# Kernel optimization log

Measured on AMD Instinct MI355X. Metric: run time of the kernel, lower is better.

## Reference

```python
import jax, jax.numpy as jnp
import numpy as np

DIM = 128
HOP = 2
NEIGH = [12, 2]  # neighbor_num per hop
ALPHA = 0.2      # leaky-relu slope
NUM_NODE = 50000
B, S = 128, 50
STDV = 1.0 / np.sqrt(DIM)


def _leaky(x):
    return jnp.where(x >= 0, x, ALPHA * x)


def _local_agg(h, adj, a_local):
    # h: [B,S,D], adj: [B,S,S] ints in 0..4, a_local: [4,D]
    a_in = h[:, :, None, :] * h[:, None, :, :]            # [B,S,S,D]
    e = _leaky(jnp.einsum('bijd,kd->kbij', a_in, a_local))  # [4,B,S,S]
    att = jnp.full(adj.shape, -9e15, dtype=h.dtype)
    for k in range(4):
        att = jnp.where(adj == k + 1, e[k], att)
    att = jax.nn.softmax(att, axis=-1)
    return jnp.einsum('bij,bjd->bid', att, h)


def _global_agg(self_v, neigh_v, extra_v, w1, w2, w3, bias):
    # self_v: [B,N,D], neigh_v: [B,N,K,D], extra_v: [B,N,D]
    a = _leaky(jnp.einsum('bnkd,de->bnke', extra_v[:, :, None, :] * neigh_v, w1))
    a = jnp.einsum('bnke,e->bnk', a, w2)
    a = jax.nn.softmax(a, axis=-1)
    agg = jnp.einsum('bnk,bnkd->bnd', a, neigh_v)
    out = jnp.concatenate([self_v, agg], axis=-1) @ w3 + bias
    return jax.nn.relu(out)


def setup_inputs() -> dict:
    key = jax.random.key(0)
    ks = jax.random.split(key, 12)
    u = lambda k, shp: jax.random.uniform(k, shp, jnp.float32, -STDV, STDV)
    return {
        'inputs': jax.random.randint(ks[0], (B, S), 0, NUM_NODE),
        'adj': jax.random.randint(ks[1], (B, S, S), 0, 5),
        'mask_item': jnp.ones((B, S), dtype=jnp.int32),
        'item': jax.random.randint(ks[2], (B, S), 0, NUM_NODE),
        'first_adj': jax.random.randint(ks[3], (B, S * NEIGH[0]), 0, NUM_NODE),
        'adj_all': jax.random.randint(ks[4], (NUM_NODE, 2), 0, NUM_NODE),
        'embedding': u(ks[5], (NUM_NODE, DIM)),
        'a_local': u(ks[6], (4, DIM)),
        'gw1': u(ks[7], (HOP, DIM, DIM)),
        'gw2': u(ks[8], (HOP, DIM)),
        'gw3': u(ks[9], (HOP, 2 * DIM, DIM)),
        'gbias': u(ks[10], (HOP, DIM)),
    }


def reference(inputs, adj, mask_item, item, first_adj, adj_all,
              embedding, a_local, gw1, gw2, gw3, gbias):
    b, s = inputs.shape
    h = embedding[inputs]                                  # [B,S,D]
    h_local = _local_agg(h, adj, a_local)

    m = mask_item.astype(embedding.dtype)[..., None]       # [B,S,1]
    item_emb = embedding[item] * m
    sum_item = jnp.sum(item_emb, 1) / jnp.sum(m, 1)        # [B,D]
    sess = sum_item[:, None, :]                            # [B,1,D]

    # multi-hop neighbor sampling
    neigh1 = first_adj.reshape(b, s * NEIGH[0])            # [B, 600]
    neigh2 = adj_all[neigh1.reshape(-1)].reshape(b, s * NEIGH[0] * NEIGH[1])  # [B,1200]
    ev = [embedding[inputs], embedding[neigh1], embedding[neigh2]]

    for n_hop in range(HOP):
        nxt = []
        for hop in range(HOP - n_hop):
            neigh_v = ev[hop + 1].reshape(b, -1, NEIGH[hop], DIM)
            extra_v = jnp.broadcast_to(sess, (b, ev[hop].shape[1], DIM))
            nxt.append(_global_agg(ev[hop], neigh_v, extra_v,
                                   gw1[n_hop], gw2[n_hop], gw3[n_hop], gbias[n_hop]))
        ev = nxt
    h_global = ev[0].reshape(b, s, DIM)

    # dropout is identity at eval
    return h_local + h_global
```

## Files before the change

kernel.cpp:

```cpp
#include <hip/hip_runtime.h>
#include <stdint.h>

typedef unsigned short ushort_t;
typedef __attribute__((ext_vector_type(8))) short bf16x8;
typedef __attribute__((ext_vector_type(4))) float f32x4;

#define B_   128
#define S_   50
#define D_   128
#define ALPHA_ 0.2f

__device__ __forceinline__ float bf2f(ushort_t u){
  return __uint_as_float(((uint32_t)u) << 16);
}
__device__ __forceinline__ ushort_t f2bf(float f){
  uint32_t x = __float_as_uint(f);
  x = (x + 0x7fffu + ((x >> 16) & 1u)) >> 16;
  return (ushort_t)x;
}
__device__ __forceinline__ float leaky(float x){ return x >= 0.f ? x : ALPHA_*x; }

__device__ __forceinline__ int detect_flag_block(const uint32_t* __restrict__ emb_raw){
  __shared__ int flg;
  if (threadIdx.x == 0){
    int ok = 1;
    for (int i = 0; i < 64; i++){
      uint32_t lo = emb_raw[i] & 0xffffu;
      uint32_t ex = (lo >> 7) & 0xFFu;
      if (!(lo == 0u || (ex >= 64u && ex <= 126u))) ok = 0;
    }
    flg = ok;
  }
  __syncthreads();
  return flg;
}

#define NLOCAL_ 512
#define NSESS_  64
#define NTPREP_ 1564
#define NCVT_   6347
#define NPREP_  48
#define TPREP_BASE_ (NLOCAL_ + NSESS_)
#define CVT_BASE_   (TPREP_BASE_ + NTPREP_)
#define PREP_BASE_  (CVT_BASE_ + NCVT_)
#define K1_GRID_    (PREP_BASE_ + NPREP_)

__global__ __launch_bounds__(256) void k1(
    const int* __restrict__ inputs, const int* __restrict__ adj,
    const int* __restrict__ item, const int* __restrict__ mask,
    const void* __restrict__ p0, const void* __restrict__ p1,
    const void* __restrict__ p2, const void* __restrict__ p3,
    const void* __restrict__ p4, const void* __restrict__ p5,
    ushort_t* __restrict__ emb_b, uint4* __restrict__ w1f, uint4* __restrict__ w3f,
    ushort_t* __restrict__ sessb, ushort_t* __restrict__ hlb,
    ushort_t* __restrict__ Tt, ushort_t* __restrict__ Tb)
{
  __shared__ uint4 smem[2048];
  int blk = blockIdx.x, tid = threadIdx.x;
  int flag = detect_flag_block((const uint32_t*)p0);

  if (blk < NLOCAL_){
    ushort_t* hSp   = (ushort_t*)smem;
    float*    attSp = (float*)((char*)smem + 17408);
    int*      sidsp = (int*)((char*)smem + 21760);
    ushort_t* alSp  = (ushort_t*)((char*)smem + 22016);
    int b  = blk >> 2;
    int mi = blk & 3;
    if (tid < 64) sidsp[tid] = (tid < S_) ? inputs[b*S_ + tid] : 0;
    for (int i = tid; i < 512; i += 256)
      alSp[i] = flag ? ((const ushort_t*)p1)[i] : f2bf(((const float*)p1)[i]);
    __syncthreads();
    if (flag){
      const ushort_t* e16 = (const ushort_t*)p0;
      for (int idx = tid; idx < 64*16; idx += 256){
        int j = idx >> 4, ch = idx & 15;
        uint4 v = {0u, 0u, 0u, 0u};
        if (j < S_) v = *(const uint4*)(e16 + (size_t)sidsp[j]*D_ + ch*8);
        *(uint4*)(hSp + j*136 + ch*8) = v;
      }
    } else {
      const float* ef = (const float*)p0;
      for (int idx = tid; idx < 64*32; idx += 256){
        int j = idx >> 5, ch = idx & 31;
        union { ushort_t u[4]; uint2 d2; } o;
        o.d2 = make_uint2(0u, 0u);
        if (j < S_){
          float4 v = *(const float4*)(ef + (size_t)sidsp[j]*D_ + ch*4);
          o.u[0]=f2bf(v.x); o.u[1]=f2bf(v.y); o.u[2]=f2bf(v.z); o.u[3]=f2bf(v.w);
        }
        *(uint2*)(hSp + j*136 + ch*4) = o.d2;
      }
    }
    for (int idx = tid; idx < 16*64; idx += 256)
      attSp[(idx >> 6)*68 + (idx & 63)] = -9.0e15f;
    __syncthreads();

    int lane = tid & 63, wv = tid >> 6;
    int q = lane >> 4, c = lane & 15;

    f32x4 Eacc[4];
    #pragma unroll
    for (int ni = 0; ni < 4; ni++) Eacc[ni] = (f32x4){0.f,0.f,0.f,0.f};
    #pragma unroll
    for (int kt = 0; kt < 4; kt++){
      uint4 av = *(const uint4*)(alSp + wv*D_ + kt*32 + q*8);
      const uint32_t* ap = (const uint32_t*)&av;
      uint4 hv = *(const uint4*)(hSp + (mi*16 + c)*136 + kt*32 + q*8);
      const uint32_t* hp = (const uint32_t*)&hv;
      union { ushort_t u[8]; bf16x8 v; } afr;
      #pragma unroll
      for (int p = 0; p < 4; p++){
        float x0 = __uint_as_float(hp[p] << 16)         * __uint_as_float(ap[p] << 16);
        float x1 = __uint_as_float(hp[p] & 0xffff0000u) * __uint_as_float(ap[p] & 0xffff0000u);
        afr.u[2*p]   = f2bf(x0);
        afr.u[2*p+1] = f2bf(x1);
      }
      #pragma unroll
      for (int ni = 0; ni < 4; ni++){
        union { uint4 q4; bf16x8 v; } bfr;
        bfr.q4 = *(const uint4*)(hSp + (ni*16 + c)*136 + kt*32 + q*8);
        Eacc[ni] = __builtin_amdgcn_mfma_f32_16x16x32_bf16(afr.v, bfr.v, Eacc[ni], 0,0,0);
      }
    }
    const int* adjb = adj + (size_t)b*S_*S_;
    #pragma unroll
    for (int ni = 0; ni < 4; ni++){
      int j = ni*16 + c;
      #pragma unroll
      for (int r = 0; r < 4; r++){
        int i = mi*16 + q*4 + r;
        if (i < S_ && j < S_){
          int kk = adjb[i*S_ + j];
          if (kk == wv + 1) attSp[(q*4 + r)*68 + j] = leaky(Eacc[ni][r]);
        }
      }
    }
    __syncthreads();
    {
      int r  = tid >> 4;
      int cg = tid & 15;
      int i  = mi*16 + r;
      float v0 = attSp[r*68 + cg*4+0], v1 = attSp[r*68 + cg*4+1];
      float v2 = attSp[r*68 + cg*4+2], v3 = attSp[r*68 + cg*4+3];
      float mx = fmaxf(fmaxf(v0,v1), fmaxf(v2,v3));
      #pragma unroll
      for (int off = 1; off < 16; off <<= 1) mx = fmaxf(mx, __shfl_xor(mx, off, 16));
      float e0 = (cg*4+0 < S_) ? __expf(v0 - mx) : 0.f;
      float e1 = (cg*4+1 < S_) ? __expf(v1 - mx) : 0.f;
      float e2 = (cg*4+2 < S_) ? __expf(v2 - mx) : 0.f;
      float e3 = (cg*4+3 < S_) ? __expf(v3 - mx) : 0.f;
      float s = e0 + e1 + e2 + e3;
      #pragma unroll
      for (int off = 1; off < 16; off <<= 1) s += __shfl_xor(s, off, 16);
      float inv = (i < S_) ? 1.f / s : 0.f;
      attSp[r*68 + cg*4+0] = e0*inv;
      attSp[r*68 + cg*4+1] = e1*inv;
      attSp[r*68 + cg*4+2] = e2*inv;
      attSp[r*68 + cg*4+3] = e3*inv;
    }
    __syncthreads();
    f32x4 Pacc[2];
    Pacc[0] = (f32x4){0.f,0.f,0.f,0.f};
    Pacc[1] = (f32x4){0.f,0.f,0.f,0.f};
    #pragma unroll
    for (int kt = 0; kt < 2; kt++){
      union { ushort_t u[8]; bf16x8 v; } afr;
      const float* arow = attSp + c*68 + kt*32 + q*8;
      #pragma unroll
      for (int j = 0; j < 8; j++) afr.u[j] = f2bf(arow[j]);
      #pragma unroll
      for (int nn = 0; nn < 2; nn++){
        int ni = 2*wv + nn;
        union { ushort_t u[8]; bf16x8 v; } bfr;
        #pragma unroll
        for (int jj = 0; jj < 8; jj++)
          bfr.u[jj] = hSp[(kt*32 + q*8 + jj)*136 + ni*16 + c];
        Pacc[nn] = __builtin_amdgcn_mfma_f32_16x16x32_bf16(afr.v, bfr.v, Pacc[nn], 0,0,0);
      }
    }
    #pragma unroll
    for (int nn = 0; nn < 2; nn++){
      int d = (2*wv + nn)*16 + c;
      #pragma unroll
      for (int r = 0; r < 4; r++){
        int i = mi*16 + q*4 + r;
        if (i < S_) hlb[((size_t)b*S_ + i)*D_ + d] = f2bf(Pacc[nn][r]);
      }
    }
  } else if (blk < NLOCAL_ + NSESS_){
    int b = (blk - NLOCAL_)*2 + (tid >> 7);
    int d = tid & 127;
    float acc = 0.f, den = 0.f;
    if (flag){
      const ushort_t* e16 = (const ushort_t*)p0;
      for (int s = 0; s < S_; s++){
        float fm = (float)mask[b*S_ + s];
        int id = item[b*S_ + s];
        acc += fm * bf2f(e16[(size_t)id*D_ + d]);
        den += fm;
      }
    } else {
      const float* ef = (const float*)p0;
      for (int s = 0; s < S_; s++){
        float fm = (float)mask[b*S_ + s];
        int id = item[b*S_ + s];
        acc += fm * ef[(size_t)id*D_ + d];
        den += fm;
      }
    }
    sessb[b*D_ + d] = f2bf(acc / den);
  } else if (blk < CVT_BASE_){
    if (!Tt) return;
    int tp   = blk - TPREP_BASE_;
    int half = tp & 1;
    int rowbase = (tp >> 1) * 64;
    for (int i = tid; i < 2048; i += 256){
      int kt = i >> 9, rem = i & 511, t = rem >> 6, ln = rem & 63;
      int q = ln >> 4, c = ln & 15;
      union { ushort_t u[8]; uint4 q4; } e;
      #pragma unroll
      for (int j = 0; j < 8; j++){
        int idx = (32*(half*4 + kt) + q*8 + j)*128 + 16*t + c;
        e.u[j] = flag ? ((const ushort_t*)p4)[idx] : f2bf(((const float*)p4)[idx]);
      }
      smem[i] = e.q4;
    }
    __syncthreads();
    int lane = tid & 63, wave = tid >> 6;
    int m = lane & 15, q = lane >> 4;
    int row = rowbase + wave*16 + m;
    int rowc = row < 50000 ? row : 49999;
    f32x4 acc[8];
    #pragma unroll
    for (int t = 0; t < 8; t++) acc[t] = (f32x4){0.f,0.f,0.f,0.f};
    #pragma unroll
    for (int kt = 0; kt < 4; kt++){
      union { ushort_t u[8]; uint4 q4; bf16x8 v; } bfr;
      if (flag){
        bfr.q4 = *(const uint4*)((const ushort_t*)p0 + (size_t)rowc*D_ + kt*32 + q*8);
      } else {
        const float* ef = (const float*)p0 + (size_t)rowc*D_ + kt*32 + q*8;
        float4 f0 = *(const float4*)(ef);
        float4 f1 = *(const float4*)(ef + 4);
        bfr.u[0]=f2bf(f0.x); bfr.u[1]=f2bf(f0.y); bfr.u[2]=f2bf(f0.z); bfr.u[3]=f2bf(f0.w);
        bfr.u[4]=f2bf(f1.x); bfr.u[5]=f2bf(f1.y); bfr.u[6]=f2bf(f1.z); bfr.u[7]=f2bf(f1.w);
      }
      #pragma unroll
      for (int t = 0; t < 8; t++){
        union { uint4 q4; bf16x8 v; } af;
        af.q4 = smem[(kt*8 + t)*64 + lane];
        acc[t] = __builtin_amdgcn_mfma_f32_16x16x32_bf16(af.v, bfr.v, acc[t], 0, 0, 0);
      }
    }
    if (row < 50000){
      ushort_t* dst = (half ? Tb : Tt) + (size_t)row*D_;
      #pragma unroll
      for (int t = 0; t < 8; t++){
        int col0 = 16*t + q*4;
        union { ushort_t u[4]; uint2 d2; } pk;
        #pragma unroll
        for (int r = 0; r < 4; r++) pk.u[r] = f2bf(acc[t][r]);
        *(uint2*)(dst + col0) = pk.d2;
      }
    }
  } else if (blk < PREP_BASE_){
    const int seg_end[6] = {6400000, 6400512, 6433280, 6433536, 6499072, 6499328};
    int base = ((blk - CVT_BASE_)*256 + tid) * 4;
    if (base >= 6499328) return;
    int s = 0;
    while (base >= seg_end[s]) s++;
    int segbase = (s == 0) ? 0 : seg_end[s-1];
    const void* src = (s==0)?p0:(s==1)?p1:(s==2)?p2:(s==3)?p3:(s==4)?p4:p5;
    int off = base - segbase;
    union { ushort_t u[4]; uint2 d2; } o;
    if (flag){
      o.d2 = *(const uint2*)((const ushort_t*)src + off);
    } else {
      float4 v = *(const float4*)((const float*)src + off);
      o.u[0] = f2bf(v.x); o.u[1] = f2bf(v.y); o.u[2] = f2bf(v.z); o.u[3] = f2bf(v.w);
    }
    *(uint2*)(emb_b + base) = o.d2;
  } else {
    int id = (blk - PREP_BASE_)*256 + tid;
    if (id >= 12288) return;
    if (id < 4096){
      int h = id >> 11, i = id & 2047;
      int kt = i >> 9, rem = i & 511, t = rem >> 6, ln = rem & 63;
      int q = ln >> 4, c = ln & 15;
      union { ushort_t u[8]; uint4 q4; } e;
      #pragma unroll
      for (int j = 0; j < 8; j++){
        int idx = h*16384 + (32*kt + q*8 + j)*128 + 16*t + c;
        e.u[j] = flag ? ((const ushort_t*)p2)[idx] : f2bf(((const float*)p2)[idx]);
      }
      w1f[h*2048 + i] = e.q4;
    } else {
      int id2 = id - 4096;
      int h = id2 >> 12, i = id2 & 4095;
      int kt = i >> 9, rem = i & 511, t = rem >> 6, ln = rem & 63;
      int q = ln >> 4, c = ln & 15;
      union { ushort_t u[8]; uint4 q4; } e;
      #pragma unroll
      for (int j = 0; j < 8; j++){
        int idx = h*32768 + (32*kt + q*8 + j)*128 + 16*t + c;
        e.u[j] = flag ? ((const ushort_t*)p4)[idx] : f2bf(((const float*)p4)[idx]);
      }
      w3f[h*4096 + i] = e.q4;
    }
  }
}

__global__ __launch_bounds__(256) void score2_ab(
    const ushort_t* __restrict__ sessb, const ushort_t* __restrict__ emb,
    const int* __restrict__ neigh1, const int* __restrict__ adj_all,
    const uint4* __restrict__ w1f, const ushort_t* __restrict__ w2,
    float* __restrict__ score)
{
  __shared__ uint4 bfrag[2048];
  __shared__ ushort_t sS[128];
  int blk = blockIdx.x, tid = threadIdx.x;
  int sb  = blk / 6;
  int sub = blk - sb*6;
  int grp = sub >> 1;
  int halft = sub & 1;
  if (tid < 16) ((uint4*)sS)[tid] = ((const uint4*)(sessb + (size_t)sb*D_))[tid];
  __syncthreads();
  for (int i = tid; i < 2048; i += 256){
    int kt = i >> 9, ln = i & 63, q = (ln >> 4);
    uint4 w = w1f[i];
    uint4 sv = *(const uint4*)(sS + kt*32 + q*8);
    const ushort_t* wu = (const ushort_t*)&w;
    const ushort_t* su = (const ushort_t*)&sv;
    union { ushort_t u[8]; uint4 q4; } o;
    #pragma unroll
    for (int j = 0; j < 8; j++) o.u[j] = f2bf(bf2f(wu[j]) * bf2f(su[j]));
    bfrag[i] = o.q4;
  }
  __syncthreads();
  int lane = tid & 63, wave = tid >> 6;
  int m = lane & 15, q = lane >> 4;
  float w2v[8];
  #pragma unroll
  for (int t = 0; t < 8; t++) w2v[t] = bf2f(w2[16*t + m]);

  int tend = halft ? 38 : 19;
  for (int t = halft*19 + wave; t < tend; t += 4){
    int rr = t*16 + m;
    int rrc = rr < 599 ? rr : 599;
    int nid;
    if (grp == 0){
      nid = neigh1[sb*600 + rrc];
    } else {
      int r2 = sb*1200 + (grp-1)*600 + rrc;
      nid = adj_all[(size_t)neigh1[r2 >> 1]*2 + (r2 & 1)];
    }
    const ushort_t* nrow = emb + (size_t)nid*D_;
    f32x4 acc[8];
    #pragma unroll
    for (int t8 = 0; t8 < 8; t8++) acc[t8] = (f32x4){0.f,0.f,0.f,0.f};
    #pragma unroll
    for (int kt = 0; kt < 4; kt++){
      union { uint4 q4; bf16x8 v; } af;
      af.q4 = *(const uint4*)(nrow + kt*32 + q*8);
      #pragma unroll
      for (int t8 = 0; t8 < 8; t8++){
        union { uint4 q4; bf16x8 v; } bf;
        bf.q4 = bfrag[(kt*8 + t8)*64 + lane];
        acc[t8] = __builtin_amdgcn_mfma_f32_16x16x32_bf16(af.v, bf.v, acc[t8], 0, 0, 0);
      }
    }
    #pragma unroll
    for (int r = 0; r < 4; r++){
      float s = 0.f;
      #pragma unroll
      for (int t8 = 0; t8 < 8; t8++) s += leaky(acc[t8][r]) * w2v[t8];
      s += __shfl_xor(s, 1, 64);
      s += __shfl_xor(s, 2, 64);
      s += __shfl_xor(s, 4, 64);
      s += __shfl_xor(s, 8, 64);
      if (m == 0){
        int rw = t*16 + q*4 + r;
        if (rw < 600){
          int sidx = (grp == 0) ? (sb*600 + rw)
                                : (76800 + sb*1200 + (grp-1)*600 + rw);
          score[sidx] = s;
        }
      }
    }
  }
}

__global__ __launch_bounds__(256) void score2_c(
    const ushort_t* __restrict__ sessb, const ushort_t* __restrict__ out1,
    const uint4* __restrict__ w1f, const ushort_t* __restrict__ w2,
    float* __restrict__ score)
{
  __shared__ uint4 bfrag[2048];
  __shared__ ushort_t sS[128];
  int blk = blockIdx.x, tid = threadIdx.x;
  int sb  = blk >> 2;
  int qtr = blk & 3;
  if (tid < 16) ((uint4*)sS)[tid] = ((const uint4*)(sessb + (size_t)sb*D_))[tid];
  __syncthreads();
  for (int i = tid; i < 2048; i += 256){
    int kt = i >> 9, ln = i & 63, q = (ln >> 4);
    uint4 w = w1f[i];
    uint4 sv = *(const uint4*)(sS + kt*32 + q*8);
    const ushort_t* wu = (const ushort_t*)&w;
    const ushort_t* su = (const ushort_t*)&sv;
    union { ushort_t u[8]; uint4 q4; } o;
    #pragma unroll
    for (int j = 0; j < 8; j++) o.u[j] = f2bf(bf2f(wu[j]) * bf2f(su[j]));
    bfrag[i] = o.q4;
  }
  __syncthreads();
  int lane = tid & 63, wave = tid >> 6;
  int m = lane & 15, q = lane >> 4;
  float w2v[8];
  #pragma unroll
  for (int t = 0; t < 8; t++) w2v[t] = bf2f(w2[16*t + m]);

  int t0 = qtr*10, tend = (qtr*10 + 10 < 38) ? qtr*10 + 10 : 38;
  for (int t = t0 + wave; t < tend; t += 4){
    int rr = t*16 + m;
    int rrc = rr < 599 ? rr : 599;
    const ushort_t* nrow = out1 + ((size_t)sb*600 + rrc)*D_;
    f32x4 acc[8];
    #pragma unroll
    for (int t8 = 0; t8 < 8; t8++) acc[t8] = (f32x4){0.f,0.f,0.f,0.f};
    #pragma unroll
    for (int kt = 0; kt < 4; kt++){
      union { uint4 q4; bf16x8 v; } af;
      af.q4 = *(const uint4*)(nrow + kt*32 + q*8);
      #pragma unroll
      for (int t8 = 0; t8 < 8; t8++){
        union { uint4 q4; bf16x8 v; } bf;
        bf.q4 = bfrag[(kt*8 + t8)*64 + lane];
        acc[t8] = __builtin_amdgcn_mfma_f32_16x16x32_bf16(af.v, bf.v, acc[t8], 0, 0, 0);
      }
    }
    #pragma unroll
    for (int r = 0; r < 4; r++){
      float s = 0.f;
      #pragma unroll
      for (int t8 = 0; t8 < 8; t8++) s += leaky(acc[t8][r]) * w2v[t8];
      s += __shfl_xor(s, 1, 64);
      s += __shfl_xor(s, 2, 64);
      s += __shfl_xor(s, 4, 64);
      s += __shfl_xor(s, 8, 64);
      if (m == 0){
        int rw = t*16 + q*4 + r;
        if (rw < 600) score[sb*600 + rw] = s;
      }
    }
  }
}

template<int K>
__device__ __forceinline__ void softmaxK(const float* __restrict__ sc, float att[K]){
  float mx = -__builtin_inff();
  #pragma unroll
  for (int k = 0; k < K; k++){ att[k] = sc[k]; mx = fmaxf(mx, att[k]); }
  float s = 0.f;
  #pragma unroll
  for (int k = 0; k < K; k++){ att[k] = __expf(att[k] - mx); s += att[k]; }
  float inv = 1.f / s;
  #pragma unroll
  for (int k = 0; k < K; k++) att[k] *= inv;
}

template<int K>
__device__ __forceinline__ void out_tile(
    int lane, const uint4* __restrict__ afrag,
    const ushort_t* __restrict__ sptr, const ushort_t* const nptr[K],
    const float att[K], f32x4 acc[8]){
  int q = lane >> 4;
  #pragma unroll
  for (int kt = 0; kt < 8; kt++){
    union { ushort_t u[8]; uint4 q4; bf16x8 v; } bfr;
    if (kt < 4){
      bfr.q4 = *(const uint4*)(sptr + kt*32 + q*8);
    } else {
      float g[8] = {0,0,0,0,0,0,0,0};
      #pragma unroll
      for (int k = 0; k < K; k++){
        uint4 nv = *(const uint4*)(nptr[k] + (kt-4)*32 + q*8);
        const uint32_t* np = (const uint32_t*)&nv;
        #pragma unroll
        for (int p = 0; p < 4; p++){
          g[2*p]   = fmaf(att[k], __uint_as_float(np[p] << 16),         g[2*p]);
          g[2*p+1] = fmaf(att[k], __uint_as_float(np[p] & 0xffff0000u), g[2*p+1]);
        }
      }
      #pragma unroll
      for (int j = 0; j < 8; j++) bfr.u[j] = f2bf(g[j]);
    }
    #pragma unroll
    for (int t = 0; t < 8; t++){
      union { uint4 q4; bf16x8 v; } af;
      af.q4 = afrag[(kt*8 + t)*64 + lane];
      acc[t] = __builtin_amdgcn_mfma_f32_16x16x32_bf16(af.v, bfr.v, acc[t], 0, 0, 0);
    }
  }
}

__global__ __launch_bounds__(256) void gather_out(
    const int* __restrict__ idx, const int* __restrict__ nbr,
    const int* __restrict__ adj_all, const float* __restrict__ score,
    const ushort_t* __restrict__ Tt, const ushort_t* __restrict__ Tb,
    const ushort_t* __restrict__ bias,
    ushort_t* __restrict__ o0c, ushort_t* __restrict__ out1c,
    int nA50, int nTot, int scoreBbase)
{
  int row  = (blockIdx.x*256 + threadIdx.x) >> 6;
  int lane = threadIdx.x & 63;
  if (row >= nTot) return;
  row = __builtin_amdgcn_readfirstlane(row);
  float b0 = bf2f(bias[lane*2]), b1 = bf2f(bias[lane*2 + 1]);
  float acc0, acc1;
  ushort_t* dst;
  if (row < nA50){
    float att[12];
    softmaxK<12>(score + (size_t)row*12, att);
    uint32_t sv = *(const uint32_t*)(Tt + (size_t)idx[row]*D_ + lane*2);
    acc0 = __uint_as_float(sv << 16);
    acc1 = __uint_as_float(sv & 0xffff0000u);
    #pragma unroll
    for (int k = 0; k < 12; k++){
      uint32_t nv = *(const uint32_t*)(Tb + (size_t)nbr[row*12 + k]*D_ + lane*2);
      acc0 = fmaf(att[k], __uint_as_float(nv << 16),          acc0);
      acc1 = fmaf(att[k], __uint_as_float(nv & 0xffff0000u),  acc1);
    }
    dst = o0c + (size_t)row*D_;
  } else {
    int rB = row - nA50;
    float att[2];
    softmaxK<2>(score + scoreBbase + (size_t)rB*2, att);
    int self = nbr[rB];
    uint32_t sv = *(const uint32_t*)(Tt + (size_t)self*D_ + lane*2);
    acc0 = __uint_as_float(sv << 16);
    acc1 = __uint_as_float(sv & 0xffff0000u);
    #pragma unroll
    for (int k = 0; k < 2; k++){
      uint32_t nv = *(const uint32_t*)(Tb + (size_t)adj_all[(size_t)self*2 + k]*D_ + lane*2);
      acc0 = fmaf(att[k], __uint_as_float(nv << 16),          acc0);
      acc1 = fmaf(att[k], __uint_as_float(nv & 0xffff0000u),  acc1);
    }
    dst = out1c + (size_t)rB*D_;
  }
  union { ushort_t u[2]; uint32_t d; } pk;
  pk.u[0] = f2bf(fmaxf(acc0 + b0, 0.f));
  pk.u[1] = f2bf(fmaxf(acc1 + b1, 0.f));
  *(uint32_t*)(dst + lane*2) = pk.d;
}

__global__ __launch_bounds__(256) void out_mfma_c2(
    const float* __restrict__ score, const ushort_t* __restrict__ out1,
    const ushort_t* __restrict__ selfsrc, const uint4* __restrict__ w3f,
    const ushort_t* __restrict__ bias,
    const ushort_t* __restrict__ addsrc, float* __restrict__ outf, int nrows){
  __shared__ uint4 afrag[4096];
  int tid = threadIdx.x;
  for (int i = tid; i < 4096; i += 256) afrag[i] = w3f[i];
  __syncthreads();
  int lane = tid & 63, wave = tid >> 6;
  int mrow = lane & 15, q = lane >> 4;
  float bv[8][4];
  #pragma unroll
  for (int t = 0; t < 8; t++){
    const ushort_t* bp = bias + 16*t + q*4;
    #pragma unroll
    for (int r = 0; r < 4; r++) bv[t][r] = bf2f(bp[r]);
  }
  int row_base = blockIdx.x*64 + wave*16;
  int row = row_base + mrow;
  bool active = row < nrows;
  int rowc = active ? row : (nrows - 1);
  const ushort_t* sptr = selfsrc + (size_t)rowc*D_;
  const ushort_t* nptr[12];
  #pragma unroll
  for (int k = 0; k < 12; k++) nptr[k] = out1 + (size_t)(rowc*12 + k)*D_;
  float att[12];
  softmaxK<12>(score + (size_t)rowc*12, att);
  f32x4 acc[8];
  #pragma unroll
  for (int t = 0; t < 8; t++) acc[t] = (f32x4){0.f,0.f,0.f,0.f};
  out_tile<12>(lane, afrag, sptr, nptr, att, acc);
  if (active){
    #pragma unroll
    for (int t = 0; t < 8; t++){
      int col0 = 16*t + q*4;
      float v[4];
      const ushort_t* ap = addsrc + (size_t)row*D_ + col0;
      #pragma unroll
      for (int r = 0; r < 4; r++)
        v[r] = fmaxf(acc[t][r] + bv[t][r], 0.f) + bf2f(ap[r]);
      *(f32x4*)(outf + (size_t)row*D_ + col0) = (f32x4){v[0], v[1], v[2], v[3]};
    }
  }
}

__global__ __launch_bounds__(256) void score_mfma_ab(
    const ushort_t* __restrict__ sessb, const ushort_t* __restrict__ emb,
    const int* __restrict__ neigh1, const int* __restrict__ adj_all,
    const uint4* __restrict__ w1f, const ushort_t* __restrict__ w2,
    float* __restrict__ score, int nA){
  __shared__ uint4 bfrag[2048];
  int tid = threadIdx.x;
  for (int i = tid; i < 2048; i += 256) bfrag[i] = w1f[i];
  __syncthreads();
  int lane = tid & 63, wave = tid >> 6;
  int m = lane & 15, q = lane >> 4;
  float w2v[8];
  #pragma unroll
  for (int t = 0; t < 8; t++) w2v[t] = bf2f(w2[16*t + m]);

  for (int it = 0; it < 2; it++){
    int row_base = blockIdx.x*128 + it*64 + wave*16;
    int row = row_base + m;
    const ushort_t* nrow; int b;
    if (row < nA){
      nrow = emb + (size_t)neigh1[row]*D_;
      b = row / 600;
    } else {
      int r2 = row - nA;
      nrow = emb + (size_t)adj_all[(size_t)neigh1[r2>>1]*2 + (r2&1)]*D_;
      b = r2 / 1200;
    }
    const ushort_t* srow = sessb + (size_t)b*D_;

    f32x4 acc[8];
    #pragma unroll
    for (int t = 0; t < 8; t++) acc[t] = (f32x4){0.f,0.f,0.f,0.f};
    #pragma unroll
    for (int kt = 0; kt < 4; kt++){
      uint4 nv = *(const uint4*)(nrow + kt*32 + q*8);
      uint4 sv = *(const uint4*)(srow + kt*32 + q*8);
      const uint32_t* np = (const uint32_t*)&nv;
      const uint32_t* sp = (const uint32_t*)&sv;
      union { ushort_t u[8]; bf16x8 v; } afr;
      #pragma unroll
      for (int p = 0; p < 4; p++){
        uint32_t n2 = np[p], s2 = sp[p];
        float a0 = __uint_as_float(n2 << 16)          * __uint_as_float(s2 << 16);
        float a1 = __uint_as_float(n2 & 0xffff0000u)  * __uint_as_float(s2 & 0xffff0000u);
        afr.u[2*p]   = f2bf(a0);
        afr.u[2*p+1] = f2bf(a1);
      }
      #pragma unroll
      for (int t = 0; t < 8; t++){
        union { uint4 q4; bf16x8 v; } bfr;
        bfr.q4 = bfrag[(kt*8 + t)*64 + lane];
        acc[t] = __builtin_amdgcn_mfma_f32_16x16x32_bf16(afr.v, bfr.v, acc[t], 0, 0, 0);
      }
    }
    #pragma unroll
    for (int r = 0; r < 4; r++){
      float s = 0.f;
      #pragma unroll
      for (int t = 0; t < 8; t++) s += leaky(acc[t][r]) * w2v[t];
      s += __shfl_xor(s, 1, 64);
      s += __shfl_xor(s, 2, 64);
      s += __shfl_xor(s, 4, 64);
      s += __shfl_xor(s, 8, 64);
      if (m == 0) score[row_base + q*4 + r] = s;
    }
  }
}

__global__ __launch_bounds__(256) void score_mfma_c(
    const ushort_t* __restrict__ sessb, const ushort_t* __restrict__ out1,
    const uint4* __restrict__ w1f, const ushort_t* __restrict__ w2,
    float* __restrict__ score){
  __shared__ uint4 bfrag[2048];
  int tid = threadIdx.x;
  for (int i = tid; i < 2048; i += 256) bfrag[i] = w1f[i];
  __syncthreads();
  int lane = tid & 63, wave = tid >> 6;
  int m = lane & 15, q = lane >> 4;
  float w2v[8];
  #pragma unroll
  for (int t = 0; t < 8; t++) w2v[t] = bf2f(w2[16*t + m]);
  for (int it = 0; it < 2; it++){
    int row_base = blockIdx.x*128 + it*64 + wave*16;
    int row = row_base + m;
    const ushort_t* nrow = out1 + (size_t)row*D_;
    int b = row / 600;
    const ushort_t* srow = sessb + (size_t)b*D_;
    f32x4 acc[8];
    #pragma unroll
    for (int t = 0; t < 8; t++) acc[t] = (f32x4){0.f,0.f,0.f,0.f};
    #pragma unroll
    for (int kt = 0; kt < 4; kt++){
      uint4 nv = *(const uint4*)(nrow + kt*32 + q*8);
      uint4 sv = *(const uint4*)(srow + kt*32 + q*8);
      const uint32_t* np = (const uint32_t*)&nv;
      const uint32_t* sp = (const uint32_t*)&sv;
      union { ushort_t u[8]; bf16x8 v; } afr;
      #pragma unroll
      for (int p = 0; p < 4; p++){
        uint32_t n2 = np[p], s2 = sp[p];
        float a0 = __uint_as_float(n2 << 16)          * __uint_as_float(s2 << 16);
        float a1 = __uint_as_float(n2 & 0xffff0000u)  * __uint_as_float(s2 & 0xffff0000u);
        afr.u[2*p]   = f2bf(a0);
        afr.u[2*p+1] = f2bf(a1);
      }
      #pragma unroll
      for (int t = 0; t < 8; t++){
        union { uint4 q4; bf16x8 v; } bfr;
        bfr.q4 = bfrag[(kt*8 + t)*64 + lane];
        acc[t] = __builtin_amdgcn_mfma_f32_16x16x32_bf16(afr.v, bfr.v, acc[t], 0, 0, 0);
      }
    }
    #pragma unroll
    for (int r = 0; r < 4; r++){
      float s = 0.f;
      #pragma unroll
      for (int t = 0; t < 8; t++) s += leaky(acc[t][r]) * w2v[t];
      s += __shfl_xor(s, 1, 64);
      s += __shfl_xor(s, 2, 64);
      s += __shfl_xor(s, 4, 64);
      s += __shfl_xor(s, 8, 64);
      if (m == 0) score[row_base + q*4 + r] = s;
    }
  }
}

__global__ __launch_bounds__(512) void out_mfma_ab(
    const float* __restrict__ score, const int* __restrict__ idx,
    const int* __restrict__ nbr, const int* __restrict__ adj_all,
    const ushort_t* __restrict__ emb, const uint4* __restrict__ w3f,
    const ushort_t* __restrict__ bias,
    ushort_t* __restrict__ o0c, ushort_t* __restrict__ out1c,
    int nA, int nTot, int scoreBbase){
  __shared__ uint4 afrag[4096];
  int tid = threadIdx.x;
  for (int i = tid; i < 4096; i += 512) afrag[i] = w3f[i];
  __syncthreads();
  int lane = tid & 63, wave = tid >> 6;
  int mrow = lane & 15, q = lane >> 4;
  float bv[8][4];
  #pragma unroll
  for (int t = 0; t < 8; t++){
    const ushort_t* bp = bias + 16*t + q*4;
    #pragma unroll
    for (int r = 0; r < 4; r++) bv[t][r] = bf2f(bp[r]);
  }
  int row_base = blockIdx.x*128 + wave*16;
  int row = row_base + mrow;
  bool active = row < nTot;
  int rowc = active ? row : (nTot - 1);
  bool isA = rowc < nA;
  f32x4 acc[8];
  #pragma unroll
  for (int t = 0; t < 8; t++) acc[t] = (f32x4){0.f,0.f,0.f,0.f};
  if (isA){
    const ushort_t* sptr = emb + (size_t)idx[rowc]*D_;
    const ushort_t* nptr[12];
    #pragma unroll
    for (int k = 0; k < 12; k++) nptr[k] = emb + (size_t)nbr[rowc*12 + k]*D_;
    float att[12];
    softmaxK<12>(score + (size_t)rowc*12, att);
    out_tile<12>(lane, afrag, sptr, nptr, att, acc);
  } else {
    int rB = rowc - nA;
    const ushort_t* sptr = emb + (size_t)nbr[rB]*D_;
    const ushort_t* nptr[2];
    #pragma unroll
    for (int k = 0; k < 2; k++) nptr[k] = emb + (size_t)adj_all[(size_t)nbr[rB]*2 + k]*D_;
    float att[2];
    softmaxK<2>(score + scoreBbase + (size_t)rB*2, att);
    out_tile<2>(lane, afrag, sptr, nptr, att, acc);
  }
  if (active){
    ushort_t* dst = isA ? (o0c + (size_t)row*D_) : (out1c + (size_t)(row - nA)*D_);
    #pragma unroll
    for (int t = 0; t < 8; t++){
      int col0 = 16*t + q*4;
      union { ushort_t u[4]; uint2 d2; } pk;
      #pragma unroll
      for (int r = 0; r < 4; r++) pk.u[r] = f2bf(fmaxf(acc[t][r] + bv[t][r], 0.f));
      *(uint2*)(dst + col0) = pk.d2;
    }
  }
}

__global__ __launch_bounds__(512) void out_mfma_c(
    const float* __restrict__ score, const ushort_t* __restrict__ out1,
    const ushort_t* __restrict__ selfsrc, const uint4* __restrict__ w3f,
    const ushort_t* __restrict__ bias,
    const ushort_t* __restrict__ addsrc, float* __restrict__ outf, int nrows){
  __shared__ uint4 afrag[4096];
  int tid = threadIdx.x;
  for (int i = tid; i < 4096; i += 512) afrag[i] = w3f[i];
  __syncthreads();
  int lane = tid & 63, wave = tid >> 6;
  int mrow = lane & 15, q = lane >> 4;
  float bv[8][4];
  #pragma unroll
  for (int t = 0; t < 8; t++){
    const ushort_t* bp = bias + 16*t + q*4;
    #pragma unroll
    for (int r = 0; r < 4; r++) bv[t][r] = bf2f(bp[r]);
  }
  int row_base = blockIdx.x*128 + wave*16;
  int row = row_base + mrow;
  bool active = row < nrows;
  int rowc = active ? row : (nrows - 1);
  const ushort_t* sptr = selfsrc + (size_t)rowc*D_;
  const ushort_t* nptr[12];
  #pragma unroll
  for (int k = 0; k < 12; k++) nptr[k] = out1 + (size_t)(rowc*12 + k)*D_;
  float att[12];
  softmaxK<12>(score + (size_t)rowc*12, att);
  f32x4 acc[8];
  #pragma unroll
  for (int t = 0; t < 8; t++) acc[t] = (f32x4){0.f,0.f,0.f,0.f};
  out_tile<12>(lane, afrag, sptr, nptr, att, acc);
  if (active){
    #pragma unroll
    for (int t = 0; t < 8; t++){
      int col0 = 16*t + q*4;
      float v[4];
      const ushort_t* ap = addsrc + (size_t)row*D_ + col0;
      #pragma unroll
      for (int r = 0; r < 4; r++)
        v[r] = fmaxf(acc[t][r] + bv[t][r], 0.f) + bf2f(ap[r]);
      *(f32x4*)(outf + (size_t)row*D_ + col0) = (f32x4){v[0], v[1], v[2], v[3]};
    }
  }
}

extern "C" void kernel_launch(void* const* d_in, const int* in_sizes, int n_in,
                              void* d_out, int out_size, void* d_ws, size_t ws_size,
                              hipStream_t stream) {
  const int* inputs    = (const int*)d_in[0];
  const int* adj       = (const int*)d_in[1];
  const int* mask_item = (const int*)d_in[2];
  const int* item      = (const int*)d_in[3];
  const int* first_adj = (const int*)d_in[4];
  const int* adj_all   = (const int*)d_in[5];

  char* ws = (char*)d_ws;
  size_t o = 0;
  ushort_t* emb_b  = (ushort_t*)(ws + o); o += 12800000;
  ushort_t* alocb  = (ushort_t*)(ws + o); o += 1024;
  ushort_t* gw1b   = (ushort_t*)(ws + o); o += 65536;
  ushort_t* gw2b   = (ushort_t*)(ws + o); o += 512;
  ushort_t* gw3b   = (ushort_t*)(ws + o); o += 131072;
  ushort_t* gbb    = (ushort_t*)(ws + o); o += 512;
  ushort_t* sessb  = (ushort_t*)(ws + o); o += 32768;
  ushort_t* hlb    = (ushort_t*)(ws + o); o += 1638400;
  uint4*    w1f    = (uint4*)(ws + o);    o += 65536;
  uint4*    w3f    = (uint4*)(ws + o);    o += 131072;
  size_t fixed = o;
  (void)alocb; (void)gw1b; (void)gw3b;

  float* outp = (float*)d_out;

  const size_t TPATH_NEED = fixed + 2*(size_t)12800000
                          + (size_t)128*153600
                          + (size_t)128*12800
                          + (size_t)3*128*600*4;
  bool tpath = (ws_size >= TPATH_NEED);

  ushort_t* Tt = nullptr; ushort_t* Tb = nullptr;
  if (tpath){
    Tt = (ushort_t*)(ws + o);  o += 12800000;
    Tb = (ushort_t*)(ws + o);  o += 12800000;
  }

  k1<<<K1_GRID_, 256, 0, stream>>>(
      inputs, adj, item, mask_item,
      d_in[6], d_in[7], d_in[8], d_in[9], d_in[10], d_in[11],
      emb_b, w1f, w3f, sessb, hlb, Tt, Tb);

  if (tpath){
    ushort_t* out1c = (ushort_t*)(ws + o);  o += (size_t)128*153600;
    ushort_t* o0c   = (ushort_t*)(ws + o);  o += (size_t)128*12800;
    float*    score = (float*)(ws + o);
    int nA600 = 128*600, nA50 = 128*50, nTot = 128*650;

    score2_ab<<<768, 256, 0, stream>>>(sessb, emb_b, first_adj, adj_all,
                                       w1f, gw2b, score);
    gather_out<<<(nTot*64 + 255)/256, 256, 0, stream>>>(inputs, first_adj, adj_all, score,
                                                        Tt, Tb, gbb, o0c, out1c,
                                                        nA50, nTot, nA600);
    score2_c<<<512, 256, 0, stream>>>(sessb, out1c, w1f + 2048, gw2b + 128, score);
    out_mfma_c2<<<(nA50 + 63)/64, 256, 0, stream>>>(score, out1c, o0c,
                                                    w3f + 4096, gbb + 128,
                                                    hlb, outp, nA50);
  } else {
    int CHB = 16;
    if      (ws_size >= fixed + (size_t)128*173600) CHB = 128;
    else if (ws_size >= fixed + (size_t)64 *173600) CHB = 64;
    else if (ws_size >= fixed + (size_t)32 *173600) CHB = 32;
    ushort_t* out1c = (ushort_t*)(ws + o);  o += (size_t)CHB*153600;
    ushort_t* o0c   = (ushort_t*)(ws + o);  o += (size_t)CHB*12800;
    float*    score = (float*)(ws + o);

    int nchunk = B_ / CHB;
    for (int c = 0; c < nchunk; c++){
      int b0 = c * CHB;
      const int* fadj  = first_adj + (size_t)b0 * 600;
      const ushort_t* sbc = sessb + (size_t)b0 * D_;
      ushort_t*  hlc   = hlb  + (size_t)b0 * 50 * D_;
      float*     outc  = outp + (size_t)b0 * 50 * D_;
      int nA600 = CHB*600, nA50 = CHB*50, nTot = CHB*650;

      score_mfma_ab<<<(3*nA600)/128, 256, 0, stream>>>(sbc, emb_b, fadj, adj_all,
                                                       w1f, gw2b, score, nA600);
      out_mfma_ab<<<(nTot + 127)/128, 512, 0, stream>>>(score, inputs + b0*50, fadj, adj_all,
                                                        emb_b, w3f, gbb, o0c, out1c,
                                                        nA50, nTot, nA600);
      score_mfma_c<<<nA600/128, 256, 0, stream>>>(sbc, out1c, w1f + 2048, gw2b + 128, score);
      out_mfma_c<<<(nA50 + 127)/128, 512, 0, stream>>>(score, out1c, o0c,
                                                       w3f + 4096, gbb + 128,
                                                       hlc, outc, nA50);
    }
  }
}
```

Before: 222.8 us.

## Move table-transform blocks into second kernel using prepacked bf16 weights and embedding

Moves the per-row embedding×W3 table precompute (Tt/Tb) out of the first fused kernel and into a new second kernel alongside the score blocks. In its new place it reads the already-converted bf16 embedding and the pre-packed w3 fragments, so it no longer reformats weights or converts fp32 per block. The conversion blocks now process 8 elements per thread with 128-bit loads, which halves the number of conversion blocks. Shared memory in the local-attention blocks becomes statically sized arrays, which may reduce per-block LDS for those blocks. In exchange, the table pass now has to wait until the whole first kernel has finished.

After: 195.4 us. -12.3%, faster.

```diff
diff --git a/kernel.cpp b/kernel.cpp
--- a/kernel.cpp
+++ b/kernel.cpp
@@ -37,11 +37,9 @@
 
 #define NLOCAL_ 512
 #define NSESS_  64
-#define NTPREP_ 1564
-#define NCVT_   6347
+#define NCVT_   3174
 #define NPREP_  48
-#define TPREP_BASE_ (NLOCAL_ + NSESS_)
-#define CVT_BASE_   (TPREP_BASE_ + NTPREP_)
+#define CVT_BASE_   (NLOCAL_ + NSESS_)
 #define PREP_BASE_  (CVT_BASE_ + NCVT_)
 #define K1_GRID_    (PREP_BASE_ + NPREP_)
 
@@ -52,31 +50,29 @@
     const void* __restrict__ p2, const void* __restrict__ p3,
     const void* __restrict__ p4, const void* __restrict__ p5,
     ushort_t* __restrict__ emb_b, uint4* __restrict__ w1f, uint4* __restrict__ w3f,
-    ushort_t* __restrict__ sessb, ushort_t* __restrict__ hlb,
-    ushort_t* __restrict__ Tt, ushort_t* __restrict__ Tb)
+    ushort_t* __restrict__ sessb, ushort_t* __restrict__ hlb)
 {
-  __shared__ uint4 smem[2048];
   int blk = blockIdx.x, tid = threadIdx.x;
   int flag = detect_flag_block((const uint32_t*)p0);
 
   if (blk < NLOCAL_){
-    ushort_t* hSp   = (ushort_t*)smem;
-    float*    attSp = (float*)((char*)smem + 17408);
-    int*      sidsp = (int*)((char*)smem + 21760);
-    ushort_t* alSp  = (ushort_t*)((char*)smem + 22016);
+    __shared__ ushort_t hS[64][136];
+    __shared__ float    attS[16][68];
+    __shared__ int      sids[64];
+    __shared__ ushort_t alS[512];
     int b  = blk >> 2;
     int mi = blk & 3;
-    if (tid < 64) sidsp[tid] = (tid < S_) ? inputs[b*S_ + tid] : 0;
+    if (tid < 64) sids[tid] = (tid < S_) ? inputs[b*S_ + tid] : 0;
     for (int i = tid; i < 512; i += 256)
-      alSp[i] = flag ? ((const ushort_t*)p1)[i] : f2bf(((const float*)p1)[i]);
+      alS[i] = flag ? ((const ushort_t*)p1)[i] : f2bf(((const float*)p1)[i]);
     __syncthreads();
     if (flag){
       const ushort_t* e16 = (const ushort_t*)p0;
       for (int idx = tid; idx < 64*16; idx += 256){
         int j = idx >> 4, ch = idx & 15;
         uint4 v = {0u, 0u, 0u, 0u};
-        if (j < S_) v = *(const uint4*)(e16 + (size_t)sidsp[j]*D_ + ch*8);
-        *(uint4*)(hSp + j*136 + ch*8) = v;
+        if (j < S_) v = *(const uint4*)(e16 + (size_t)sids[j]*D_ + ch*8);
+        *(uint4*)(&hS[j][ch*8]) = v;
       }
     } else {
       const float* ef = (const float*)p0;
@@ -85,14 +81,14 @@
         union { ushort_t u[4]; uint2 d2; } o;
         o.d2 = make_uint2(0u, 0u);
         if (j < S_){
-          float4 v = *(const float4*)(ef + (size_t)sidsp[j]*D_ + ch*4);
+          float4 v = *(const float4*)(ef + (size_t)sids[j]*D_ + ch*4);
           o.u[0]=f2bf(v.x); o.u[1]=f2bf(v.y); o.u[2]=f2bf(v.z); o.u[3]=f2bf(v.w);
         }
-        *(uint2*)(hSp + j*136 + ch*4) = o.d2;
+        *(uint2*)(&hS[j][ch*4]) = o.d2;
       }
     }
     for (int idx = tid; idx < 16*64; idx += 256)
-      attSp[(idx >> 6)*68 + (idx & 63)] = -9.0e15f;
+      attS[idx >> 6][idx & 63] = -9.0e15f;
     __syncthreads();
 
     int lane = tid & 63, wv = tid >> 6;
@@ -103,9 +99,9 @@
     for (int ni = 0; ni < 4; ni++) Eacc[ni] = (f32x4){0.f,0.f,0.f,0.f};
     #pragma unroll
     for (int kt = 0; kt < 4; kt++){
-      uint4 av = *(const uint4*)(alSp + wv*D_ + kt*32 + q*8);
+      uint4 av = *(const uint4*)(alS + wv*D_ + kt*32 + q*8);
       const uint32_t* ap = (const uint32_t*)&av;
-      uint4 hv = *(const uint4*)(hSp + (mi*16 + c)*136 + kt*32 + q*8);
+      uint4 hv = *(const uint4*)(&hS[mi*16 + c][kt*32 + q*8]);
       const uint32_t* hp = (const uint32_t*)&hv;
       union { ushort_t u[8]; bf16x8 v; } afr;
       #pragma unroll
@@ -118,7 +114,7 @@
       #pragma unroll
       for (int ni = 0; ni < 4; ni++){
         union { uint4 q4; bf16x8 v; } bfr;
-        bfr.q4 = *(const uint4*)(hSp + (ni*16 + c)*136 + kt*32 + q*8);
+        bfr.q4 = *(const uint4*)(&hS[ni*16 + c][kt*32 + q*8]);
         Eacc[ni] = __builtin_amdgcn_mfma_f32_16x16x32_bf16(afr.v, bfr.v, Eacc[ni], 0,0,0);
       }
     }
@@ -131,7 +127,7 @@
         int i = mi*16 + q*4 + r;
         if (i < S_ && j < S_){
           int kk = adjb[i*S_ + j];
-          if (kk == wv + 1) attSp[(q*4 + r)*68 + j] = leaky(Eacc[ni][r]);
+          if (kk == wv + 1) attS[q*4 + r][j] = leaky(Eacc[ni][r]);
         }
       }
     }
@@ -140,8 +136,8 @@
       int r  = tid >> 4;
       int cg = tid & 15;
       int i  = mi*16 + r;
-      float v0 = attSp[r*68 + cg*4+0], v1 = attSp[r*68 + cg*4+1];
-      float v2 = attSp[r*68 + cg*4+2], v3 = attSp[r*68 + cg*4+3];
+      float v0 = attS[r][cg*4+0], v1 = attS[r][cg*4+1];
+      float v2 = attS[r][cg*4+2], v3 = attS[r][cg*4+3];
       float mx = fmaxf(fmaxf(v0,v1), fmaxf(v2,v3));
       #pragma unroll
       for (int off = 1; off < 16; off <<= 1) mx = fmaxf(mx, __shfl_xor(mx, off, 16));
@@ -153,10 +149,10 @@
       #pragma unroll
       for (int off = 1; off < 16; off <<= 1) s += __shfl_xor(s, off, 16);
       float inv = (i < S_) ? 1.f / s : 0.f;
-      attSp[r*68 + cg*4+0] = e0*inv;
-      attSp[r*68 + cg*4+1] = e1*inv;
-      attSp[r*68 + cg*4+2] = e2*inv;
-      attSp[r*68 + cg*4+3] = e3*inv;
+      attS[r][cg*4+0] = e0*inv;
+      attS[r][cg*4+1] = e1*inv;
+      attS[r][cg*4+2] = e2*inv;
+      attS[r][cg*4+3] = e3*inv;
     }
     __syncthreads();
     f32x4 Pacc[2];
@@ -165,7 +161,7 @@
     #pragma unroll
     for (int kt = 0; kt < 2; kt++){
       union { ushort_t u[8]; bf16x8 v; } afr;
-      const float* arow = attSp + c*68 + kt*32 + q*8;
+      const float* arow = &attS[c][kt*32 + q*8];
       #pragma unroll
       for (int j = 0; j < 8; j++) afr.u[j] = f2bf(arow[j]);
       #pragma unroll
@@ -174,7 +170,7 @@
         union { ushort_t u[8]; bf16x8 v; } bfr;
         #pragma unroll
         for (int jj = 0; jj < 8; jj++)
-          bfr.u[jj] = hSp[(kt*32 + q*8 + jj)*136 + ni*16 + c];
+          bfr.u[jj] = hS[kt*32 + q*8 + jj][ni*16 + c];
         Pacc[nn] = __builtin_amdgcn_mfma_f32_16x16x32_bf16(afr.v, bfr.v, Pacc[nn], 0,0,0);
       }
     }
@@ -187,7 +183,7 @@
         if (i < S_) hlb[((size_t)b*S_ + i)*D_ + d] = f2bf(Pacc[nn][r]);
       }
     }
-  } else if (blk < NLOCAL_ + NSESS_){
+  } else if (blk < CVT_BASE_){
     int b = (blk - NLOCAL_)*2 + (tid >> 7);
     int d = tid & 127;
     float acc = 0.f, den = 0.f;
@@ -209,77 +205,26 @@
       }
     }
     sessb[b*D_ + d] = f2bf(acc / den);
-  } else if (blk < CVT_BASE_){
-    if (!Tt) return;
-    int tp   = blk - TPREP_BASE_;
-    int half = tp & 1;
-    int rowbase = (tp >> 1) * 64;
-    for (int i = tid; i < 2048; i += 256){
-      int kt = i >> 9, rem = i & 511, t = rem >> 6, ln = rem & 63;
-      int q = ln >> 4, c = ln & 15;
-      union { ushort_t u[8]; uint4 q4; } e;
-      #pragma unroll
-      for (int j = 0; j < 8; j++){
-        int idx = (32*(half*4 + kt) + q*8 + j)*128 + 16*t + c;
-        e.u[j] = flag ? ((const ushort_t*)p4)[idx] : f2bf(((const float*)p4)[idx]);
-      }
-      smem[i] = e.q4;
-    }
-    __syncthreads();
-    int lane = tid & 63, wave = tid >> 6;
-    int m = lane & 15, q = lane >> 4;
-    int row = rowbase + wave*16 + m;
-    int rowc = row < 50000 ? row : 49999;
-    f32x4 acc[8];
-    #pragma unroll
-    for (int t = 0; t < 8; t++) acc[t] = (f32x4){0.f,0.f,0.f,0.f};
-    #pragma unroll
-    for (int kt = 0; kt < 4; kt++){
-      union { ushort_t u[8]; uint4 q4; bf16x8 v; } bfr;
-      if (flag){
-        bfr.q4 = *(const uint4*)((const ushort_t*)p0 + (size_t)rowc*D_ + kt*32 + q*8);
-      } else {
-        const float* ef = (const float*)p0 + (size_t)rowc*D_ + kt*32 + q*8;
-        float4 f0 = *(const float4*)(ef);
-        float4 f1 = *(const float4*)(ef + 4);
-        bfr.u[0]=f2bf(f0.x); bfr.u[1]=f2bf(f0.y); bfr.u[2]=f2bf(f0.z); bfr.u[3]=f2bf(f0.w);
-        bfr.u[4]=f2bf(f1.x); bfr.u[5]=f2bf(f1.y); bfr.u[6]=f2bf(f1.z); bfr.u[7]=f2bf(f1.w);
-      }
-      #pragma unroll
-      for (int t = 0; t < 8; t++){
-        union { uint4 q4; bf16x8 v; } af;
-        af.q4 = smem[(kt*8 + t)*64 + lane];
-        acc[t] = __builtin_amdgcn_mfma_f32_16x16x32_bf16(af.v, bfr.v, acc[t], 0, 0, 0);
-      }
-    }
-    if (row < 50000){
-      ushort_t* dst = (half ? Tb : Tt) + (size_t)row*D_;
-      #pragma unroll
-      for (int t = 0; t < 8; t++){
-        int col0 = 16*t + q*4;
-        union { ushort_t u[4]; uint2 d2; } pk;
-        #pragma unroll
-        for (int r = 0; r < 4; r++) pk.u[r] = f2bf(acc[t][r]);
-        *(uint2*)(dst + col0) = pk.d2;
-      }
-    }
   } else if (blk < PREP_BASE_){
     const int seg_end[6] = {6400000, 6400512, 6433280, 6433536, 6499072, 6499328};
-    int base = ((blk - CVT_BASE_)*256 + tid) * 4;
+    int base = ((blk - CVT_BASE_)*256 + tid) * 8;
     if (base >= 6499328) return;
     int s = 0;
     while (base >= seg_end[s]) s++;
     int segbase = (s == 0) ? 0 : seg_end[s-1];
     const void* src = (s==0)?p0:(s==1)?p1:(s==2)?p2:(s==3)?p3:(s==4)?p4:p5;
     int off = base - segbase;
-    union { ushort_t u[4]; uint2 d2; } o;
+    union { ushort_t u[8]; uint4 q4; } o;
     if (flag){
-      o.d2 = *(const uint2*)((const ushort_t*)src + off);
+      o.q4 = *(const uint4*)((const ushort_t*)src + off);
     } else {
-      float4 v = *(const float4*)((const float*)src + off);
-      o.u[0] = f2bf(v.x); o.u[1] = f2bf(v.y); o.u[2] = f2bf(v.z); o.u[3] = f2bf(v.w);
-    }
-    *(uint2*)(emb_b + base) = o.d2;
+      const float* fp = (const float*)src + off;
+      float4 v0 = *(const float4*)(fp);
+      float4 v1 = *(const float4*)(fp + 4);
+      o.u[0]=f2bf(v0.x); o.u[1]=f2bf(v0.y); o.u[2]=f2bf(v0.z); o.u[3]=f2bf(v0.w);
+      o.u[4]=f2bf(v1.x); o.u[5]=f2bf(v1.y); o.u[6]=f2bf(v1.z); o.u[7]=f2bf(v1.w);
+    }
+    *(uint4*)(emb_b + base) = o.q4;
   } else {
     int id = (blk - PREP_BASE_)*256 + tid;
     if (id >= 12288) return;
@@ -310,17 +255,62 @@
   }
 }
 
-__global__ __launch_bounds__(256) void score2_ab(
-    const ushort_t* __restrict__ sessb, const ushort_t* __restrict__ emb,
+#define NT2TPREP_ 1564
+#define NT2SCORE_ 768
+#define K2_GRID_  (NT2TPREP_ + NT2SCORE_)
+
+__global__ __launch_bounds__(256) void k2(
+    const ushort_t* __restrict__ emb, const uint4* __restrict__ w3f,
+    ushort_t* __restrict__ Tt, ushort_t* __restrict__ Tb,
+    const ushort_t* __restrict__ sessb,
     const int* __restrict__ neigh1, const int* __restrict__ adj_all,
     const uint4* __restrict__ w1f, const ushort_t* __restrict__ w2,
     float* __restrict__ score)
 {
-  __shared__ uint4 bfrag[2048];
+  __shared__ uint4 frag[2048];
   __shared__ ushort_t sS[128];
   int blk = blockIdx.x, tid = threadIdx.x;
-  int sb  = blk / 6;
-  int sub = blk - sb*6;
+
+  if (blk < NT2TPREP_){
+    int half = blk & 1;
+    int rowbase = (blk >> 1) * 64;
+    for (int i = tid; i < 2048; i += 256) frag[i] = w3f[half*2048 + i];
+    __syncthreads();
+    int lane = tid & 63, wave = tid >> 6;
+    int m = lane & 15, q = lane >> 4;
+    int row = rowbase + wave*16 + m;
+    int rowc = row < 50000 ? row : 49999;
+    f32x4 acc[8];
+    #pragma unroll
+    for (int t = 0; t < 8; t++) acc[t] = (f32x4){0.f,0.f,0.f,0.f};
+    #pragma unroll
+    for (int kt = 0; kt < 4; kt++){
+      union { uint4 q4; bf16x8 v; } bfr;
+      bfr.q4 = *(const uint4*)(emb + (size_t)rowc*D_ + kt*32 + q*8);
+      #pragma unroll
+      for (int t = 0; t < 8; t++){
+        union { uint4 q4; bf16x8 v; } af;
+        af.q4 = frag[(kt*8 + t)*64 + lane];
+        acc[t] = __builtin_amdgcn_mfma_f32_16x16x32_bf16(af.v, bfr.v, acc[t], 0, 0, 0);
+      }
+    }
+    if (row < 50000){
+      ushort_t* dst = (half ? Tb : Tt) + (size_t)row*D_;
+      #pragma unroll
+      for (int t = 0; t < 8; t++){
+        int col0 = 16*t + q*4;
+        union { ushort_t u[4]; uint2 d2; } pk;
+        #pragma unroll
+        for (int r = 0; r < 4; r++) pk.u[r] = f2bf(acc[t][r]);
+        *(uint2*)(dst + col0) = pk.d2;
+      }
+    }
+    return;
+  }
+
+  int b2  = blk - NT2TPREP_;
+  int sb  = b2 / 6;
+  int sub = b2 - sb*6;
   int grp = sub >> 1;
   int halft = sub & 1;
   if (tid < 16) ((uint4*)sS)[tid] = ((const uint4*)(sessb + (size_t)sb*D_))[tid];
@@ -334,7 +324,7 @@
     union { ushort_t u[8]; uint4 q4; } o;
     #pragma unroll
     for (int j = 0; j < 8; j++) o.u[j] = f2bf(bf2f(wu[j]) * bf2f(su[j]));
-    bfrag[i] = o.q4;
+    frag[i] = o.q4;
   }
   __syncthreads();
   int lane = tid & 63, wave = tid >> 6;
@@ -365,7 +355,7 @@
       #pragma unroll
       for (int t8 = 0; t8 < 8; t8++){
         union { uint4 q4; bf16x8 v; } bf;
-        bf.q4 = bfrag[(kt*8 + t8)*64 + lane];
+        bf.q4 = frag[(kt*8 + t8)*64 + lane];
         acc[t8] = __builtin_amdgcn_mfma_f32_16x16x32_bf16(af.v, bf.v, acc[t8], 0, 0, 0);
       }
     }
@@ -864,25 +854,22 @@
                           + (size_t)3*128*600*4;
   bool tpath = (ws_size >= TPATH_NEED);
 
-  ushort_t* Tt = nullptr; ushort_t* Tb = nullptr;
-  if (tpath){
-    Tt = (ushort_t*)(ws + o);  o += 12800000;
-    Tb = (ushort_t*)(ws + o);  o += 12800000;
-  }
-
   k1<<<K1_GRID_, 256, 0, stream>>>(
       inputs, adj, item, mask_item,
       d_in[6], d_in[7], d_in[8], d_in[9], d_in[10], d_in[11],
-      emb_b, w1f, w3f, sessb, hlb, Tt, Tb);
+      emb_b, w1f, w3f, sessb, hlb);
 
   if (tpath){
+    ushort_t* Tt    = (ushort_t*)(ws + o);  o += 12800000;
+    ushort_t* Tb    = (ushort_t*)(ws + o);  o += 12800000;
     ushort_t* out1c = (ushort_t*)(ws + o);  o += (size_t)128*153600;
     ushort_t* o0c   = (ushort_t*)(ws + o);  o += (size_t)128*12800;
     float*    score = (float*)(ws + o);
     int nA600 = 128*600, nA50 = 128*50, nTot = 128*650;
 
-    score2_ab<<<768, 256, 0, stream>>>(sessb, emb_b, first_adj, adj_all,
-                                       w1f, gw2b, score);
+    k2<<<K2_GRID_, 256, 0, stream>>>(emb_b, w3f, Tt, Tb,
+                                     sessb, first_adj, adj_all,
+                                     w1f, gw2b, score);
     gather_out<<<(nTot*64 + 255)/256, 256, 0, stream>>>(inputs, first_adj, adj_all, score,
                                                         Tt, Tb, gbb, o0c, out1c,
                                                         nA50, nTot, nA600);
```
